# Performance work log

Measured on AMD Instinct MI355X. Metric: run time of the kernel, lower is better.

## Reference

```python
import jax, jax.numpy as jnp
import numpy as np


def _conv1x1(x, W, b):
    # x: [B,C,H,W] (NCHW), W: [out,in] (1x1 conv kernel), b: [out]
    return jnp.einsum('bchw,oc->bohw', x, W) + b[None, :, None, None]


def setup_inputs() -> dict:
    key = jax.random.key(0)
    ks = jax.random.split(key, 12)
    B, C, H, W = 8, 256, 64, 64
    s = 1.0 / np.sqrt(C)
    x = jax.random.normal(ks[0], (B, C, H, W), dtype=jnp.float32)
    mask = jnp.round(jax.random.uniform(ks[1], (B, 1, H, W), dtype=jnp.float32))
    Wq = jax.random.normal(ks[2], (C, C), dtype=jnp.float32) * s
    bq = jax.random.normal(ks[3], (C,), dtype=jnp.float32) * 0.01
    Wk = jax.random.normal(ks[4], (C, C), dtype=jnp.float32) * s
    bk = jax.random.normal(ks[5], (C,), dtype=jnp.float32) * 0.01
    Wv = jax.random.normal(ks[6], (C, C), dtype=jnp.float32) * s
    bv = jax.random.normal(ks[7], (C,), dtype=jnp.float32) * 0.01
    Wo = jax.random.normal(ks[8], (C, C), dtype=jnp.float32) * s
    bo = jax.random.normal(ks[9], (C,), dtype=jnp.float32) * 0.01
    gamma = jnp.zeros((1,), dtype=jnp.float32)
    return {"input": x, "mask": mask, "Wq": Wq, "bq": bq, "Wk": Wk, "bk": bk,
            "Wv": Wv, "bv": bv, "Wo": Wo, "bo": bo, "gamma": gamma}


def reference(input, mask, Wq, bq, Wk, bk, Wv, bv, Wo, bo, gamma):
    B, C, H, W = input.shape
    # mask spatial size matches input -> no avg_pool branch (pre_feat is None)
    feat_f = input * mask            # foreground features -> queries
    feat_b = input * (1.0 - mask)    # background features -> keys/values
    q = _conv1x1(feat_f, Wq, bq).reshape(B, C, -1)   # [B,C,N]
    k = _conv1x1(feat_b, Wk, bk).reshape(B, C, -1)   # [B,C,N]
    v = _conv1x1(feat_b, Wv, bv).reshape(B, C, -1)   # [B,C,N]
    # scores[b,n,m] = q[:,n]^T k[:,m]  (no scaling, matching the torch code)
    scores = jnp.einsum('bcn,bcm->bnm', q, k)        # [B,N,N]
    attn = jax.nn.softmax(scores, axis=-1)
    out = jnp.einsum('bnm,bcm->bcn', attn, v).reshape(B, C, H, W)
    out = _conv1x1(out, Wo, bo)
    return out + gamma * input
```

## Files before the change

kernel.cpp:

```cpp
#include <hip/hip_runtime.h>

#define CC 256
#define NN 4096
#define NB 8
#define NM ((size_t)CC * NN)

#define OFF_OVF   589824
#define OFF_LM    720896
#define OFF_POSM  739328
#define OFF_POSF  747520
#define OFF_CNT   755712
#define OFF_W16   755776
#define PMAIN     524288
#define QCAP      2304

typedef _Float16 f16;
typedef f16 f16x4 __attribute__((ext_vector_type(4)));
typedef f16 f16x8 __attribute__((ext_vector_type(8)));
typedef float f32x4 __attribute__((ext_vector_type(4)));
typedef unsigned int u32;

#define GLD16(gp, lp) __builtin_amdgcn_global_load_lds( \
    (const __attribute__((address_space(1))) u32*)(const void*)(gp), \
    (__attribute__((address_space(3))) u32*)(void*)(lp), 16, 0, 0)

__global__ __launch_bounds__(256) void wprep_kernel(
    const float* __restrict__ Wq, const float* __restrict__ Wk,
    const float* __restrict__ Wv, const float* __restrict__ Wo,
    f16* __restrict__ w16)
{
    int i = (blockIdx.x * 256 + threadIdx.x) * 4;
    float4 a = *(const float4*)(Wq + i);
    float4 b = *(const float4*)(Wk + i);
    float4 c = *(const float4*)(Wv + i);
    float4 d = *(const float4*)(Wo + i);
    f16x4 ha, hb, hc, hd;
    ha[0]=(f16)a.x; ha[1]=(f16)a.y; ha[2]=(f16)a.z; ha[3]=(f16)a.w;
    hb[0]=(f16)b.x; hb[1]=(f16)b.y; hb[2]=(f16)b.z; hb[3]=(f16)b.w;
    hc[0]=(f16)c.x; hc[1]=(f16)c.y; hc[2]=(f16)c.z; hc[3]=(f16)c.w;
    hd[0]=(f16)d.x; hd[1]=(f16)d.y; hd[2]=(f16)d.z; hd[3]=(f16)d.w;
    *(f16x4*)(w16 + i)            = ha;
    *(f16x4*)(w16 + 65536 + i)    = hb;
    *(f16x4*)(w16 + 131072 + i)   = hc;
    *(f16x4*)(w16 + 196608 + i)   = hd;
}

__global__ __launch_bounds__(256) void mask_scan_kernel(
    const float* __restrict__ mask, f16* __restrict__ wsh, int b0)
{
    const int slot = blockIdx.x;
    const int b = b0 + slot;
    const int t = threadIdx.x;
    const int lane = t & 63, w = t >> 6;
    __shared__ int wsum0[4], wsum1[4];
    const float* mp = mask + (size_t)b * NN;
    f16* base = wsh + (size_t)slot * 4 * NM;
    int* pm = (int*)(base + OFF_POSM);
    int* pf = (int*)(base + OFF_POSF);
    int* cn = (int*)(base + OFF_CNT);

    int loc0[16], loc1[16], c0 = 0, c1 = 0;
    float mv[16];
#pragma unroll
    for (int i = 0; i < 16; ++i) {
        mv[i] = mp[t * 16 + i];
        loc0[i] = c0; loc1[i] = c1;
        if (mv[i] == 0.0f) ++c0; else ++c1;
    }
    int i0 = c0, i1 = c1;
#pragma unroll
    for (int d = 1; d < 64; d <<= 1) {
        int v0 = __shfl_up(i0, d, 64);
        int v1 = __shfl_up(i1, d, 64);
        if (lane >= d) { i0 += v0; i1 += v1; }
    }
    if (lane == 63) { wsum0[w] = i0; wsum1[w] = i1; }
    int e0 = i0 - c0, e1 = i1 - c1;
    __syncthreads();
    int s0 = e0, s1 = e1;
    for (int i = 0; i < w; ++i) { s0 += wsum0[i]; s1 += wsum1[i]; }
#pragma unroll
    for (int i = 0; i < 16; ++i) {
        pm[t * 16 + i] = (mv[i] == 0.0f) ? (s0 + loc0[i]) : -1;
        pf[t * 16 + i] = (mv[i] != 0.0f) ? (s1 + loc1[i]) : -1;
    }
    if (t == 0) {
        cn[0] = wsum0[0] + wsum0[1] + wsum0[2] + wsum0[3];
        cn[1] = wsum1[0] + wsum1[1] + wsum1[2] + wsum1[3];
    }
}

__global__ __launch_bounds__(512, 4) void proj_fused_kernel(
    const float* __restrict__ x, const float* __restrict__ mask,
    const f16* __restrict__ w16, const float* __restrict__ bq,
    const float* __restrict__ bk, const float* __restrict__ bv,
    f16* __restrict__ wsh, int b0)
{
    __shared__ f16x8 xf[2048];
    __shared__ f16x8 xb[2048];

    const int t = threadIdx.x;
    const int lane = t & 63, w = t >> 6;
    const int l16 = lane & 15, quad = lane >> 4;
    const int slot = blockIdx.x;
    const int b = b0 + slot;
    const int n0 = blockIdx.y * 64;
    const float* xp = x + (size_t)b * NM;
    f16* base = wsh + (size_t)slot * 4 * NM;
    const int* pom = (const int*)(base + OFF_POSM);
    const int* pof = (const int*)(base + OFF_POSF);
    const int* cn  = (const int*)(base + OFF_CNT);

    float mf  = mask[(size_t)b * NN + n0 + lane];
    float mbk = 1.0f - mf;
#pragma unroll
    for (int i = 0; i < 4; ++i) {
        int cb = w * 4 + i;
        const float* col = xp + (size_t)cb * 8 * NN + n0 + lane;
        f16x8 vf, vb;
#pragma unroll
        for (int u = 0; u < 8; ++u) {
            float xv = col[(size_t)u * NN];
            vf[u] = (f16)(xv * mf);
            vb[u] = (f16)(xv * mbk);
        }
        int unit = ((cb >> 2) * 4 + (lane >> 4)) * 64 + (cb & 3) * 16 + (lane & 15);
        xf[unit] = vf;
        xb[unit] = vb;
    }
    __syncthreads();

#pragma unroll
    for (int pr = 0; pr < 3; ++pr) {
        int j0  = w * 6 + pr * 2;
        int p   = j0 >> 4;
        int oc0 = j0 & 15;
        const f16* Wp     = w16 + (size_t)p * 65536;
        const float* bias = (p == 0) ? bq : (p == 1) ? bk : bv;
        const f16x8* bt   = (p == 0) ? xf : xb;

        f16x8 wf[2][8];
#pragma unroll
        for (int h = 0; h < 2; ++h) {
            const f16* wrow = Wp + (size_t)((oc0 + h) * 16 + l16) * CC + quad * 8;
#pragma unroll
            for (int kc = 0; kc < 8; ++kc)
                wf[h][kc] = *(const f16x8*)(wrow + kc * 32);
        }
        f32x4 acc[2][4];
#pragma unroll
        for (int h = 0; h < 2; ++h)
#pragma unroll
            for (int nc = 0; nc < 4; ++nc) acc[h][nc] = (f32x4){0.f, 0.f, 0.f, 0.f};
#pragma unroll
        for (int nc = 0; nc < 4; ++nc)
#pragma unroll
            for (int kc = 0; kc < 8; ++kc) {
                f16x8 bf = bt[(kc * 4 + nc) * 64 + lane];
                acc[0][nc] = __builtin_amdgcn_mfma_f32_16x16x32_f16(wf[0][kc], bf, acc[0][nc], 0, 0, 0);
                acc[1][nc] = __builtin_amdgcn_mfma_f32_16x16x32_f16(wf[1][kc], bf, acc[1][nc], 0, 0, 0);
            }
#pragma unroll
        for (int h = 0; h < 2; ++h) {
            int oc = oc0 + h;
            float bvv[4];
#pragma unroll
            for (int r = 0; r < 4; ++r) bvv[r] = bias[oc * 16 + quad * 4 + r];
            if (p == 2) {
                f16* vpl = base + 2 * NM;
#pragma unroll
                for (int nc = 0; nc < 4; ++nc) {
                    int cp = pom[n0 + nc * 16 + l16];
                    if (cp >= 0) {
#pragma unroll
                        for (int r = 0; r < 4; ++r)
                            vpl[(size_t)(oc * 16 + quad * 4 + r) * NN + cp] =
                                (f16)(acc[h][nc][r] + bvv[r]);
                    }
                }
            } else if (p == 1) {
                f16* kpl = base + NM;
#pragma unroll
                for (int nc = 0; nc < 4; ++nc) {
                    int cp = pom[n0 + nc * 16 + l16];
                    if (cp >= 0) {
                        f16x4 pk;
#pragma unroll
                        for (int r = 0; r < 4; ++r) pk[r] = (f16)(acc[h][nc][r] + bvv[r]);
                        *(f16x4*)(kpl + (size_t)cp * CC + oc * 16 + quad * 4) = pk;
                    }
                }
            } else {
#pragma unroll
                for (int nc = 0; nc < 4; ++nc) {
                    int cp = pof[n0 + nc * 16 + l16];
                    if (cp >= 0) {
                        f16x4 pk;
#pragma unroll
                        for (int r = 0; r < 4; ++r) pk[r] = (f16)(acc[h][nc][r] + bvv[r]);
                        *(f16x4*)(base + (size_t)cp * CC + oc * 16 + quad * 4) = pk;
                    }
                }
            }
        }
    }

    if (blockIdx.y == 0) {
        int Fb = cn[0], Ff = cn[1];
        f16x8 z8;
#pragma unroll
        for (int i = 0; i < 8; ++i) z8[i] = (f16)0.0f;
        {
            int Mp = (Fb + 31) & ~31;
            int pad = Mp - Fb;
            if (pad > 0) {
                f16* kpl = base + NM;
                f16* vpl = base + 2 * NM;
                for (int idx = t; idx < pad * 32; idx += 512)
                    *(f16x8*)(kpl + (size_t)(Fb + idx / 32) * CC + (idx & 31) * 8) = z8;
                for (int idx = t; idx < pad * CC; idx += 512)
                    vpl[(size_t)(idx / pad) * NN + Fb + (idx % pad)] = (f16)0.0f;
            }
        }
        for (int c = t; c < CC; c += 512)
            base[(size_t)Ff * CC + c] = (f16)bq[c];
        {
            int qe = (Ff + 64) & ~63;
            int nz = qe - (Ff + 1);
            for (int idx = t; idx < nz * 32; idx += 512)
                *(f16x8*)(base + (size_t)(Ff + 1 + idx / 32) * CC + (idx & 31) * 8) = z8;
        }
    }
}

__global__ __launch_bounds__(256, 4) void flash_kernel(
    f16* __restrict__ wsh, const float* __restrict__ bk,
    const float* __restrict__ bv, int b0)
{
    __shared__ f16x8 klds[1024];
    __shared__ f16x8 vlds[1024];
    __shared__ f16 pbuf[4][16 * 40];

    const int t    = threadIdx.x;
    const int w    = t >> 6;
    const int lane = t & 63;
    const int l16  = lane & 15;
    const int quad = lane >> 4;
    const int slot = blockIdx.x;
    const int n0   = (blockIdx.y >> 1) * 64;
    const int z    = blockIdx.y & 1;

    f16* base = wsh + (size_t)slot * 4 * NM;
    const int* cn = (const int*)(base + OFF_CNT);
    const int Fb = cn[0], Ff = cn[1];
    if (n0 > Ff) return;

    const f16* qt = base;
    const f16* kt = base + NM;
    const f16* vp = base + 2 * NM;

    const int nt  = (Fb + 31) >> 5;
    const int h   = (nt + 1) >> 1;
    const int mt0 = z ? h : 0;
    const int mt1 = z ? nt : h;

    int koff[4], voff[4];
#pragma unroll
    for (int i = 0; i < 4; ++i) {
        int u = i * 256 + t;
        koff[i] = (((u >> 9) & 1) * 16 + (u & 15)) * CC
                + ((u >> 6) & 7) * 32 + ((u >> 4) & 3) * 8;
        voff[i] = ((u >> 6) * 16 + (u & 15)) * NN + ((u >> 4) & 3) * 8;
    }

#define ISSUE(m0_) do {                                                         \
    _Pragma("unroll")                                                           \
    for (int i_ = 0; i_ < 4; ++i_)                                              \
        GLD16(kt + (size_t)(m0_) * CC + koff[i_],                               \
              (f16*)&klds[i_ * 256 + w * 64]);                                  \
    _Pragma("unroll")                                                           \
    for (int i_ = 0; i_ < 4; ++i_)                                              \
        GLD16(vp + (size_t)(m0_) + voff[i_],                                    \
              (f16*)&vlds[i_ * 256 + w * 64]);                                  \
} while (0)

    const int nrow = n0 + w * 16 + l16;
    f16x8 qf[8];
#pragma unroll
    for (int kc = 0; kc < 8; ++kc)
        qf[kc] = *(const f16x8*)(qt + (size_t)nrow * CC + kc * 32 + quad * 8);
#pragma unroll
    for (int kc = 0; kc < 8; ++kc)
        asm volatile("" :: "v"(qf[kc]));
    asm volatile("s_waitcnt vmcnt(0)" ::: "memory");

    f32x4 oacc[17];
#pragma unroll
    for (int i = 0; i < 17; ++i) oacc[i] = (f32x4){0.f, 0.f, 0.f, 0.f};
    float M[4] = {-3.0e38f, -3.0e38f, -3.0e38f, -3.0e38f};

    f16* pw = &pbuf[w][0];
    f16x8 ones;
#pragma unroll
    for (int i = 0; i < 8; ++i) ones[i] = (f16)1.0f;

    for (int it = mt0; it < mt1; ++it) {
        ISSUE(it * 32);
        asm volatile("s_waitcnt vmcnt(0)" ::: "memory");
        __builtin_amdgcn_s_barrier();
        asm volatile("" ::: "memory");

        f32x4 s[2];
        s[0] = (f32x4){0.f, 0.f, 0.f, 0.f};
        s[1] = (f32x4){0.f, 0.f, 0.f, 0.f};
        __builtin_amdgcn_s_setprio(1);
#pragma unroll
        for (int kc = 0; kc < 8; ++kc) {
            f16x8 k0 = klds[kc * 64 + lane];
            f16x8 k1 = klds[(8 + kc) * 64 + lane];
            s[0] = __builtin_amdgcn_mfma_f32_16x16x32_f16(qf[kc], k0, s[0], 0, 0, 0);
            s[1] = __builtin_amdgcn_mfma_f32_16x16x32_f16(qf[kc], k1, s[1], 0, 0, 0);
        }
        __builtin_amdgcn_s_setprio(0);

        if (((it + 1) << 5) > Fb) {
#pragma unroll
            for (int ms = 0; ms < 2; ++ms)
                if (it * 32 + ms * 16 + l16 >= Fb) {
#pragma unroll
                    for (int r = 0; r < 4; ++r) s[ms][r] = -3.0e38f;
                }
        }

        bool up = false;
#pragma unroll
        for (int ms = 0; ms < 2; ++ms)
#pragma unroll
            for (int r = 0; r < 4; ++r) up |= (s[ms][r] > M[r] + 8.0f);
        if (__any(up)) {
            float alpha[4];
#pragma unroll
            for (int r = 0; r < 4; ++r) {
                float tm = fmaxf(s[0][r], s[1][r]);
                tm = fmaxf(tm, __shfl_xor(tm, 1, 64));
                tm = fmaxf(tm, __shfl_xor(tm, 2, 64));
                tm = fmaxf(tm, __shfl_xor(tm, 4, 64));
                tm = fmaxf(tm, __shfl_xor(tm, 8, 64));
                float Mn = fmaxf(M[r], tm);
                alpha[r] = __expf(M[r] - Mn);
                M[r] = Mn;
            }
#pragma unroll
            for (int cs = 0; cs < 17; ++cs)
#pragma unroll
                for (int r = 0; r < 4; ++r) oacc[cs][r] *= alpha[r];
        }
#pragma unroll
        for (int ms = 0; ms < 2; ++ms)
#pragma unroll
            for (int r = 0; r < 4; ++r)
                pw[(quad * 4 + r) * 40 + ms * 16 + l16] = (f16)__expf(s[ms][r] - M[r]);
        asm volatile("s_waitcnt lgkmcnt(0)" ::: "memory");
        f16x8 pf = *(const f16x8*)(pw + l16 * 40 + quad * 8);

        __builtin_amdgcn_s_setprio(1);
#pragma unroll
        for (int cs = 0; cs < 16; ++cs) {
            f16x8 vf = vlds[cs * 64 + lane];
            oacc[cs] = __builtin_amdgcn_mfma_f32_16x16x32_f16(pf, vf, oacc[cs], 0, 0, 0);
        }
        oacc[16] = __builtin_amdgcn_mfma_f32_16x16x32_f16(pf, ones, oacc[16], 0, 0, 0);
        __builtin_amdgcn_s_setprio(0);

        asm volatile("" ::: "memory");
        __builtin_amdgcn_s_barrier();
    }
    asm volatile("s_waitcnt vmcnt(0)" ::: "memory");

    if (z == 0) {
        float cnn = 0.f;
#pragma unroll
        for (int kc = 0; kc < 8; ++kc) {
            const float* bkp = bk + kc * 32 + quad * 8;
#pragma unroll
            for (int j = 0; j < 8; ++j)
                cnn += (float)qf[kc][j] * bkp[j];
        }
        cnn += __shfl_xor(cnn, 16, 64);
        cnn += __shfl_xor(cnn, 32, 64);
        const float Ffw = (float)Ff;
        float aw[4], wv[4];
#pragma unroll
        for (int r = 0; r < 4; ++r) {
            float cr = __shfl(cnn, quad * 4 + r, 64);
            float Mn = fmaxf(M[r], cr);
            aw[r] = __expf(M[r] - Mn);
            wv[r] = Ffw * __expf(cr - Mn);
            M[r] = Mn;
        }
#pragma unroll
        for (int cs = 0; cs < 16; ++cs) {
            float bvc = bv[cs * 16 + l16];
#pragma unroll
            for (int r = 0; r < 4; ++r)
                oacc[cs][r] = oacc[cs][r] * aw[r] + wv[r] * bvc;
        }
#pragma unroll
        for (int r = 0; r < 4; ++r)
            oacc[16][r] = oacc[16][r] * aw[r] + wv[r];
    }

    float inv[4];
#pragma unroll
    for (int r = 0; r < 4; ++r) {
        float Lr = oacc[16][r];
        inv[r] = (Lr > 0.f) ? 1.0f / Lr : 0.f;
    }
#pragma unroll
    for (int r = 0; r < 4; ++r) {
        int row = n0 + w * 16 + quad * 4 + r;
        f16* pp = (row < 2048)
                ? base + 3 * NM + (size_t)z * PMAIN + (size_t)row * 256
                : base + OFF_OVF + (size_t)z * 65536 + (size_t)(row - 2048) * 256;
#pragma unroll
        for (int cs = 0; cs < 16; ++cs)
            pp[cs * 16 + l16] = (f16)(oacc[cs][r] * inv[r]);
    }
    if (l16 == 0) {
        float* LMw = (float*)(base + OFF_LM);
#pragma unroll
        for (int r = 0; r < 4; ++r) {
            int row = n0 + w * 16 + quad * 4 + r;
            LMw[((size_t)z * QCAP + row) * 2 + 0] = oacc[16][r];
            LMw[((size_t)z * QCAP + row) * 2 + 1] = M[r];
        }
    }
#undef ISSUE
}

__global__ __launch_bounds__(256, 2) void combine_kernel(
    const f16* __restrict__ wsh, const float* __restrict__ bo,
    const float* __restrict__ x, const float* __restrict__ gamma,
    float* __restrict__ outall, int b0)
{
    __shared__ f16x8 ot[2048];

    const int t = threadIdx.x;
    const int lane = t & 63, w = t >> 6;
    const int l16 = lane & 15, quad = lane >> 4;
    const int slot = blockIdx.x;
    const int b = b0 + slot;
    const int n0 = blockIdx.y * 64;

    const f16* base = wsh + (size_t)slot * 4 * NM;
    const int* pof = (const int*)(base + OFF_POSF);
    const int* cn  = (const int*)(base + OFF_CNT);
    const int Ff = cn[1];
    const float* LMp = (const float*)(base + OFF_LM);
    const f16* wo16 = wsh + OFF_W16 + (size_t)3 * 65536;

#pragma unroll
    for (int i = 0; i < 8; ++i) {
        int u = i * 256 + t;
        int ul16 = u & 15, uq = (u >> 4) & 3, unc = (u >> 6) & 3, ukc = u >> 8;
        int orign = n0 + unc * 16 + ul16;
        int pfv = pof[orign];
        int crow = (pfv >= 0) ? pfv : Ff;
        int c0 = ukc * 32 + uq * 8;
        const f16* p0 = (crow < 2048)
                      ? base + 3 * NM + (size_t)crow * 256
                      : base + OFF_OVF + (size_t)(crow - 2048) * 256;
        const f16* p1 = (crow < 2048)
                      ? base + 3 * NM + PMAIN + (size_t)crow * 256
                      : base + OFF_OVF + 65536 + (size_t)(crow - 2048) * 256;
        f16x8 o0 = *(const f16x8*)(p0 + c0);
        f16x8 o1 = *(const f16x8*)(p1 + c0);
        float L0 = LMp[(size_t)crow * 2], M0 = LMp[(size_t)crow * 2 + 1];
        float L1 = LMp[((size_t)QCAP + crow) * 2], M1 = LMp[((size_t)QCAP + crow) * 2 + 1];
        float Mx = fmaxf(M0, M1);
        float w0 = L0 * __expf(M0 - Mx);
        float w1 = L1 * __expf(M1 - Mx);
        float inv = 1.0f / (w0 + w1);
        f16x8 om;
#pragma unroll
        for (int j = 0; j < 8; ++j)
            om[j] = (f16)((w0 * (float)o0[j] + w1 * (float)o1[j]) * inv);
        ot[u] = om;
    }
    __syncthreads();

    const float* xp = x + (size_t)b * NM;
    float* outp = outall + (size_t)b * NM;
    float g = gamma[0];
#pragma unroll
    for (int pr = 0; pr < 2; ++pr) {
        int oc0 = w * 4 + pr * 2;
        f16x8 wf[2][8];
#pragma unroll
        for (int h = 0; h < 2; ++h) {
            const f16* wrow = wo16 + (size_t)((oc0 + h) * 16 + l16) * CC + quad * 8;
#pragma unroll
            for (int kc = 0; kc < 8; ++kc)
                wf[h][kc] = *(const f16x8*)(wrow + kc * 32);
        }
        f32x4 acc[2][4];
#pragma unroll
        for (int h = 0; h < 2; ++h)
#pragma unroll
            for (int nc = 0; nc < 4; ++nc) acc[h][nc] = (f32x4){0.f, 0.f, 0.f, 0.f};
#pragma unroll
        for (int nc = 0; nc < 4; ++nc)
#pragma unroll
            for (int kc = 0; kc < 8; ++kc) {
                f16x8 bf = ot[(kc * 4 + nc) * 64 + lane];
                acc[0][nc] = __builtin_amdgcn_mfma_f32_16x16x32_f16(wf[0][kc], bf, acc[0][nc], 0, 0, 0);
                acc[1][nc] = __builtin_amdgcn_mfma_f32_16x16x32_f16(wf[1][kc], bf, acc[1][nc], 0, 0, 0);
            }
#pragma unroll
        for (int h = 0; h < 2; ++h) {
            int oc = oc0 + h;
            float bvv[4];
#pragma unroll
            for (int r = 0; r < 4; ++r) bvv[r] = bo[oc * 16 + quad * 4 + r];
#pragma unroll
            for (int nc = 0; nc < 4; ++nc)
#pragma unroll
                for (int r = 0; r < 4; ++r) {
                    size_t o = oc * 16 + quad * 4 + r;
                    size_t n = n0 + nc * 16 + l16;
                    outp[o * NN + n] = acc[h][nc][r] + bvv[r] + g * xp[o * NN + n];
                }
        }
    }
}

__global__ __launch_bounds__(256) void ones_kernel(float* __restrict__ out, int total)
{
    for (int i = blockIdx.x * 256 + threadIdx.x; i < total; i += gridDim.x * 256)
        out[i] = 1.0f;
}

extern "C" void kernel_launch(void* const* d_in, const int* in_sizes, int n_in,
                              void* d_out, int out_size, void* d_ws, size_t ws_size,
                              hipStream_t stream)
{
    const float* x     = (const float*)d_in[0];
    const float* mask  = (const float*)d_in[1];
    const float* Wq    = (const float*)d_in[2];
    const float* bq    = (const float*)d_in[3];
    const float* Wk    = (const float*)d_in[4];
    const float* bk    = (const float*)d_in[5];
    const float* Wv    = (const float*)d_in[6];
    const float* bv    = (const float*)d_in[7];
    const float* Wo    = (const float*)d_in[8];
    const float* bo    = (const float*)d_in[9];
    const float* gamma = (const float*)d_in[10];
    float* out = (float*)d_out;

    const size_t slot_bytes = 4 * NM * sizeof(f16);
    f16* wsh = (f16*)d_ws;
    int nb = (int)(ws_size / slot_bytes);
    if (nb < 1) {
        ones_kernel<<<2048, 256, 0, stream>>>(out, out_size);
        return;
    }
    if (nb > NB) nb = NB;

    f16* w16 = wsh + OFF_W16;
    wprep_kernel<<<64, 256, 0, stream>>>(Wq, Wk, Wv, Wo, w16);

    for (int b0 = 0; b0 < NB; b0 += nb) {
        int nbc = NB - b0; if (nbc > nb) nbc = nb;
        mask_scan_kernel<<<nbc, 256, 0, stream>>>(mask, wsh, b0);
        dim3 gP(nbc, NN / 64);
        dim3 gF(nbc, (QCAP / 64) * 2);
        dim3 gC(nbc, NN / 64);
        proj_fused_kernel<<<gP, 512, 0, stream>>>(x, mask, w16, bq, bk, bv, wsh, b0);
        flash_kernel<<<gF, 256, 0, stream>>>(wsh, bk, bv, b0);
        combine_kernel<<<gC, 256, 0, stream>>>(wsh, bo, x, gamma, out, b0);
    }
}
```

Measured before the change: 300.0 us.

## Register-prefetch next K/V tile in flash loop instead of direct LDS loads

Replaces the synchronous global_load_lds issue-then-wait per iteration with a register double-buffer. The next K/V tile is loaded into registers while the current tile's MFMAs run, then written to LDS at the top of the next iteration. Launch bounds occupancy drops from 4 to 2 waves per SIMD to make room for the extra registers. The aim is to hide global load latency behind compute, at the cost of lower occupancy and extra VGPR-to-LDS store traffic.

```diff
diff --git a/kernel.cpp b/kernel.cpp
--- a/kernel.cpp
+++ b/kernel.cpp
@@ -19,10 +19,6 @@
 typedef f16 f16x8 __attribute__((ext_vector_type(8)));
 typedef float f32x4 __attribute__((ext_vector_type(4)));
 typedef unsigned int u32;
-
-#define GLD16(gp, lp) __builtin_amdgcn_global_load_lds( \
-    (const __attribute__((address_space(1))) u32*)(const void*)(gp), \
-    (__attribute__((address_space(3))) u32*)(void*)(lp), 16, 0, 0)
 
 __global__ __launch_bounds__(256) void wprep_kernel(
     const float* __restrict__ Wq, const float* __restrict__ Wk,
@@ -233,7 +229,7 @@
     }
 }
 
-__global__ __launch_bounds__(256, 4) void flash_kernel(
+__global__ __launch_bounds__(256, 2) void flash_kernel(
     f16* __restrict__ wsh, const float* __restrict__ bk,
     const float* __restrict__ bv, int b0)
 {
@@ -273,26 +269,11 @@
         voff[i] = ((u >> 6) * 16 + (u & 15)) * NN + ((u >> 4) & 3) * 8;
     }
 
-#define ISSUE(m0_) do {                                                         \
-    _Pragma("unroll")                                                           \
-    for (int i_ = 0; i_ < 4; ++i_)                                              \
-        GLD16(kt + (size_t)(m0_) * CC + koff[i_],                               \
-              (f16*)&klds[i_ * 256 + w * 64]);                                  \
-    _Pragma("unroll")                                                           \
-    for (int i_ = 0; i_ < 4; ++i_)                                              \
-        GLD16(vp + (size_t)(m0_) + voff[i_],                                    \
-              (f16*)&vlds[i_ * 256 + w * 64]);                                  \
-} while (0)
-
     const int nrow = n0 + w * 16 + l16;
     f16x8 qf[8];
 #pragma unroll
     for (int kc = 0; kc < 8; ++kc)
         qf[kc] = *(const f16x8*)(qt + (size_t)nrow * CC + kc * 32 + quad * 8);
-#pragma unroll
-    for (int kc = 0; kc < 8; ++kc)
-        asm volatile("" :: "v"(qf[kc]));
-    asm volatile("s_waitcnt vmcnt(0)" ::: "memory");
 
     f32x4 oacc[17];
 #pragma unroll
@@ -304,11 +285,29 @@
 #pragma unroll
     for (int i = 0; i < 8; ++i) ones[i] = (f16)1.0f;
 
+    f16x8 kreg[4], vreg[4];
+    if (mt1 > mt0) {
+#pragma unroll
+        for (int i = 0; i < 4; ++i) {
+            kreg[i] = *(const f16x8*)(kt + (size_t)(mt0 * 32) * CC + koff[i]);
+            vreg[i] = *(const f16x8*)(vp + (size_t)(mt0 * 32) + voff[i]);
+        }
+    }
+
     for (int it = mt0; it < mt1; ++it) {
-        ISSUE(it * 32);
-        asm volatile("s_waitcnt vmcnt(0)" ::: "memory");
-        __builtin_amdgcn_s_barrier();
-        asm volatile("" ::: "memory");
+#pragma unroll
+        for (int i = 0; i < 4; ++i) {
+            klds[i * 256 + t] = kreg[i];
+            vlds[i * 256 + t] = vreg[i];
+        }
+        __syncthreads();
+        if (it + 1 < mt1) {
+#pragma unroll
+            for (int i = 0; i < 4; ++i) {
+                kreg[i] = *(const f16x8*)(kt + (size_t)((it + 1) * 32) * CC + koff[i]);
+                vreg[i] = *(const f16x8*)(vp + (size_t)((it + 1) * 32) + voff[i]);
+            }
+        }
 
         f32x4 s[2];
         s[0] = (f32x4){0.f, 0.f, 0.f, 0.f};
@@ -372,10 +371,8 @@
         oacc[16] = __builtin_amdgcn_mfma_f32_16x16x32_f16(pf, ones, oacc[16], 0, 0, 0);
         __builtin_amdgcn_s_setprio(0);
 
-        asm volatile("" ::: "memory");
-        __builtin_amdgcn_s_barrier();
-    }
-    asm volatile("s_waitcnt vmcnt(0)" ::: "memory");
+        __syncthreads();
+    }
 
     if (z == 0) {
         float cnn = 0.f;
@@ -435,7 +432,6 @@
             LMw[((size_t)z * QCAP + row) * 2 + 1] = M[r];
         }
     }
-#undef ISSUE
 }
 
 __global__ __launch_bounds__(256, 2) void combine_kernel(
```

Result: faster. 278.8 us (-7.1%).
